# Kernel tuning notes

Hardware: AMD Instinct MI355X
Metric: run time of the kernel (lower is better)

## Reference

```python
import jax, jax.numpy as jnp
import numpy as np

DIM = 384
HEADS = 6
EPS = 1e-5
SCALE = DIM ** -0.5  # note: original uses full dim, not head_dim


def _dwconv_bn(x, w, stride, g, b, m, v):
    # x: [B, C, H, W], w: [C, 1, 3, 3] depthwise
    y = jax.lax.conv_general_dilated(
        x, w, window_strides=(stride, stride), padding=((1, 1), (1, 1)),
        dimension_numbers=('NCHW', 'OIHW', 'NCHW'), feature_group_count=DIM)
    # BatchNorm2d inference form
    inv = jax.lax.rsqrt(v + EPS)
    y = (y - m[None, :, None, None]) * (inv * g)[None, :, None, None] + b[None, :, None, None]
    # b c h w -> b (h w) c
    B, C, H, W = y.shape
    return y.reshape(B, C, H * W).transpose(0, 2, 1)


def setup_inputs() -> dict:
    key = jax.random.key(0)
    ks = jax.random.split(key, 24)
    d = {}
    d['x'] = jax.random.normal(ks[0], (8, 3136, DIM), jnp.float32)
    d['h'] = 56
    d['w'] = 56
    i = 1
    for nm in ('q', 'k', 'v'):
        d[f'conv_{nm}'] = jax.random.normal(ks[i], (DIM, 1, 3, 3), jnp.float32) * 0.1; i += 1
        d[f'bn{nm}_s'] = jnp.ones((DIM,), jnp.float32)
        d[f'bn{nm}_b'] = jnp.zeros((DIM,), jnp.float32)
        d[f'bn{nm}_m'] = jax.random.normal(ks[i], (DIM,), jnp.float32) * 0.1; i += 1
        d[f'bn{nm}_v'] = jax.random.uniform(ks[i], (DIM,), jnp.float32) + 0.5; i += 1
    s = DIM ** -0.5
    d['wq'] = jax.random.normal(ks[i], (DIM, DIM), jnp.float32) * s; i += 1
    d['wk'] = jax.random.normal(ks[i], (DIM, DIM), jnp.float32) * s; i += 1
    d['wv'] = jax.random.normal(ks[i], (DIM, DIM), jnp.float32) * s; i += 1
    d['w_last'] = jax.random.normal(ks[i], (DIM, DIM), jnp.float32) * s; i += 1
    d['b_last'] = jnp.zeros((DIM,), jnp.float32)
    return d


def reference(x, h, w, conv_q, bnq_s, bnq_b, bnq_m, bnq_v,
              conv_k, bnk_s, bnk_b, bnk_m, bnk_v,
              conv_v, bnv_s, bnv_b, bnv_m, bnv_v,
              wq, wk, wv, w_last, b_last):
    B, T, C = x.shape
    xim = x.transpose(0, 2, 1).reshape(B, C, h, w)  # b (h w) c -> b c h w
    q = _dwconv_bn(xim, conv_q, 1, bnq_s, bnq_b, bnq_m, bnq_v)  # [B, h*w, C]
    k = _dwconv_bn(xim, conv_k, 2, bnk_s, bnk_b, bnk_m, bnk_v)  # [B, hw/4, C]
    v = _dwconv_bn(xim, conv_v, 2, bnv_s, bnv_b, bnv_m, bnv_v)
    # linear projections (torch Linear: y = x @ W.T), split heads
    def heads(t, W):
        y = jnp.einsum('btc,oc->bto', t, W)
        Bt, Tt, _ = y.shape
        return y.reshape(Bt, Tt, HEADS, C // HEADS).transpose(0, 2, 1, 3)
    qh, kh, vh = heads(q, wq), heads(k, wk), heads(v, wv)
    attn = jax.nn.softmax(jnp.einsum('bhld,bhtd->bhlt', qh, kh) * SCALE, axis=-1)
    o = jnp.einsum('bhlt,bhtd->bhld', attn, vh)  # [B, H, L, d]
    o = o.transpose(0, 2, 1, 3).reshape(B, T, C)
    return jnp.einsum('btc,oc->bto', o, w_last) + b_last
```

## Files before the change

### kernel.cpp

```cpp
#include <hip/hip_runtime.h>
#include <hip/hip_bf16.h>

typedef __bf16 bf16;
typedef __attribute__((ext_vector_type(8))) __bf16 bf16x8;
typedef __attribute__((ext_vector_type(4))) __bf16 bf16x4;
typedef __attribute__((ext_vector_type(4))) float floatx4;

#define MFMA16(a, b, c) __builtin_amdgcn_mfma_f32_16x16x32_bf16((a), (b), (c), 0, 0, 0)

#define DIM 384
#define T1 3136
#define T2 784
#define T2P 832
#define B_ 8
#define EPSV 1e-5f

__device__ __forceinline__ void gload_lds16(const bf16* g, bf16* l) {
  __builtin_amdgcn_global_load_lds(
      (const __attribute__((address_space(1))) void*)g,
      (__attribute__((address_space(3))) void*)l, 16, 0, 0);
}

__global__ void conv_fused_kernel(const float* __restrict__ x,
    const float* __restrict__ wqc, const float* __restrict__ gq, const float* __restrict__ bq,
    const float* __restrict__ mq, const float* __restrict__ vq,
    const float* __restrict__ wkc, const float* __restrict__ gk, const float* __restrict__ bk,
    const float* __restrict__ mk, const float* __restrict__ vk,
    const float* __restrict__ wvc, const float* __restrict__ gv, const float* __restrict__ bv,
    const float* __restrict__ mv, const float* __restrict__ vvv,
    bf16* __restrict__ qout, bf16* __restrict__ kout, bf16* __restrict__ vout,
    const float* __restrict__ w0, const float* __restrict__ w1,
    const float* __restrict__ w2, const float* __restrict__ w3,
    bf16* __restrict__ d0, bf16* __restrict__ d1,
    bf16* __restrict__ d2, bf16* __restrict__ d3) {
  int blk = blockIdx.x;
  int c = threadIdx.x;
  int gid = blk * DIM + c;
  if (gid < 147456) {
    d0[gid] = (bf16)w0[gid]; d1[gid] = (bf16)w1[gid];
    d2[gid] = (bf16)w2[gid]; d3[gid] = (bf16)w3[gid];
  }
  int xg = blk % 14;
  int y = (blk / 14) % 56;
  int b = blk / (14 * 56);
  int x0 = xg * 4;
  const float* xb = x + (size_t)b * T1 * DIM;
  float in[3][6];
#pragma unroll
  for (int r = 0; r < 3; ++r) {
    int yy = y + r - 1;
#pragma unroll
    for (int cc = 0; cc < 6; ++cc) {
      int xc = x0 + cc - 1;
      in[r][cc] = (yy >= 0 && yy < 56 && xc >= 0 && xc < 56)
                      ? xb[(yy * 56 + xc) * DIM + c] : 0.f;
    }
  }
  {
    float wr[9];
#pragma unroll
    for (int i = 0; i < 9; ++i) wr[i] = wqc[c * 9 + i];
    float a = rsqrtf(vq[c] + EPSV) * gq[c];
    float bia = bq[c] - mq[c] * a;
#pragma unroll
    for (int p = 0; p < 4; ++p) {
      float s = 0.f;
#pragma unroll
      for (int r = 0; r < 3; ++r)
#pragma unroll
        for (int dx = 0; dx < 3; ++dx) s += in[r][p + dx] * wr[r * 3 + dx];
      qout[((size_t)b * T1 + y * 56 + x0 + p) * DIM + c] = (bf16)(s * a + bia);
    }
  }
  if ((y & 1) == 0) {
    int y2 = y >> 1;
    float wk9[9], wv9[9];
#pragma unroll
    for (int i = 0; i < 9; ++i) { wk9[i] = wkc[c * 9 + i]; wv9[i] = wvc[c * 9 + i]; }
    float ak = rsqrtf(vk[c] + EPSV) * gk[c];
    float av = rsqrtf(vvv[c] + EPSV) * gv[c];
    float bik = bk[c] - mk[c] * ak;
    float biv = bv[c] - mv[c] * av;
#pragma unroll
    for (int p2 = 0; p2 < 2; ++p2) {
      float sk = 0.f, sv = 0.f;
#pragma unroll
      for (int r = 0; r < 3; ++r)
#pragma unroll
        for (int dx = 0; dx < 3; ++dx) {
          float xv = in[r][2 * p2 + dx];
          sk += xv * wk9[r * 3 + dx];
          sv += xv * wv9[r * 3 + dx];
        }
      size_t o = ((size_t)b * T2 + y2 * 28 + (x0 >> 1) + p2) * DIM + c;
      kout[o] = (bf16)(sk * ak + bik);
      vout[o] = (bf16)(sv * av + biv);
    }
  }
}

#define BK 32
__device__ __forceinline__
void gemm_body(const bf16* A, const bf16* Bw, void* out, const float* bias,
               int mode, float scale, int m0, int n0, bf16* Al, bf16* Bl) {
  int tid = threadIdx.x;
  int w = tid >> 6, lane = tid & 63;
  int wm = w >> 1, wn = w & 1;
  int l16 = lane & 15, quad = lane >> 4;
  floatx4 acc[4][4];
#pragma unroll
  for (int i = 0; i < 4; ++i)
#pragma unroll
    for (int j = 0; j < 4; ++j) acc[i][j] = (floatx4){0.f, 0.f, 0.f, 0.f};

  int srow = w * 32 + (lane >> 2);
  int scol = (lane & 3) * 8;
  const bf16* ag0 = &A[(size_t)(m0 + srow) * DIM + scol];
  const bf16* ag1 = ag0 + (size_t)16 * DIM;
  const bf16* bg0 = &Bw[(size_t)(n0 + srow) * DIM + scol];
  const bf16* bg1 = bg0 + (size_t)16 * DIM;
  bf16* la0 = &Al[(w * 32) * BK];
  bf16* la1 = &Al[(w * 32 + 16) * BK];
  bf16* lb0 = &Bl[(w * 32) * BK];
  bf16* lb1 = &Bl[(w * 32 + 16) * BK];

  for (int k0 = 0; k0 < DIM; k0 += BK) {
    __syncthreads();
    gload_lds16(ag0 + k0, la0);
    gload_lds16(ag1 + k0, la1);
    gload_lds16(bg0 + k0, lb0);
    gload_lds16(bg1 + k0, lb1);
    __syncthreads();
    bf16x8 af[4], bfr[4];
#pragma unroll
    for (int i = 0; i < 4; ++i) {
      af[i]  = *(const bf16x8*)&Al[(wm * 64 + i * 16 + l16) * BK + quad * 8];
      bfr[i] = *(const bf16x8*)&Bl[(wn * 64 + i * 16 + l16) * BK + quad * 8];
    }
#pragma unroll
    for (int i = 0; i < 4; ++i)
#pragma unroll
      for (int j = 0; j < 4; ++j)
        acc[i][j] = MFMA16(af[i], bfr[j], acc[i][j]);
  }
#pragma unroll
  for (int i = 0; i < 4; ++i) {
#pragma unroll
    for (int j = 0; j < 4; ++j) {
#pragma unroll
      for (int rr = 0; rr < 4; ++rr) {
        int row = m0 + wm * 64 + i * 16 + quad * 4 + rr;
        int col = n0 + wn * 64 + j * 16 + l16;
        float v = acc[i][j][rr];
        if (mode == 3) {
          ((float*)out)[(size_t)row * DIM + col] = v + bias[col];
        } else if (mode == 2) {
          int b = row / T2;
          int t = row - b * T2;
          ((bf16*)out)[((size_t)b * DIM + col) * T2P + t] = (bf16)v;
        } else {
          ((bf16*)out)[(size_t)row * DIM + col] = (bf16)(v * scale);
        }
      }
    }
  }
}

__global__ __launch_bounds__(256)
void qkv_gemm_kernel(const bf16* q_act, const bf16* k_act, const bf16* v_act,
                     const bf16* wqb, const bf16* wkb, const bf16* wvb,
                     bf16* Qp, bf16* Kp, bf16* Vtp, float qscale) {
  __shared__ bf16 Al[128 * BK];
  __shared__ bf16 Bl[128 * BK];
  int bx = blockIdx.x;
  int xp = bx & 7, j = bx >> 3;
  int t = (j / 3) * 24 + xp * 3 + (j % 3);
  if (t >= 882) return;
  const bf16 *A, *Bw; void* out; int mode, ti; float scale;
  if (t < 588)      { A = q_act; Bw = wqb; out = Qp;  mode = 1; scale = qscale; ti = t; }
  else if (t < 735) { A = k_act; Bw = wkb; out = Kp;  mode = 0; scale = 1.f; ti = t - 588; }
  else              { A = v_act; Bw = wvb; out = Vtp; mode = 2; scale = 1.f; ti = t - 735; }
  gemm_body(A, Bw, out, nullptr, mode, scale, (ti / 3) * 128, (ti % 3) * 128, Al, Bl);
}

__global__ __launch_bounds__(256)
void last_gemm_kernel(const bf16* A, const bf16* Bw, float* out, const float* bias) {
  __shared__ bf16 Al[128 * BK];
  __shared__ bf16 Bl[128 * BK];
  int bx = blockIdx.x;
  int xp = bx & 7, j = bx >> 3;
  int t = (j / 3) * 24 + xp * 3 + (j % 3);
  if (t >= 588) return;
  gemm_body(A, Bw, out, bias, 3, 1.f, (t / 3) * 128, (t % 3) * 128, Al, Bl);
}

__global__ __launch_bounds__(256, 4)
void attn_kernel(const bf16* __restrict__ Qp, const bf16* __restrict__ Kp,
                 const bf16* __restrict__ Vt, bf16* __restrict__ Ob) {
  __shared__ bf16 Kl[64 * 64];
  __shared__ bf16 Vl[64 * 64];
  __shared__ bf16 Pl[4][2][16 * 64];
  int bx = blockIdx.x;
  int xcd = bx & 7, j = bx >> 3;
  int g = xcd + 8 * (j / 25);
  int qblk = j % 25;
  int h = g % 6;
  int b = g / 6;
  int tid = threadIdx.x, w = tid >> 6, lane = tid & 63;
  int l16 = lane & 15, quad = lane >> 4;
  int q0w = qblk * 128 + w * 32;

  bf16x8 qf[2][2];
#pragma unroll
  for (int qt = 0; qt < 2; ++qt) {
    int qi = q0w + qt * 16 + l16;
    qi = qi < T1 ? qi : T1 - 1;
    const bf16* qp = &Qp[((size_t)b * T1 + qi) * DIM + h * 64];
    qf[qt][0] = *(const bf16x8*)&qp[quad * 8];
    qf[qt][1] = *(const bf16x8*)&qp[32 + quad * 8];
  }
  floatx4 oacc[2][4];
#pragma unroll
  for (int qt = 0; qt < 2; ++qt)
#pragma unroll
    for (int dt = 0; dt < 4; ++dt) oacc[qt][dt] = (floatx4){0.f, 0.f, 0.f, 0.f};
  float lsum[2] = {0.f, 0.f};

  int rsub = lane >> 3;
  int chnk = (lane & 7) ^ rsub;
  const bf16* kg0 = &Kp[((size_t)b * T2 + w * 16 + rsub) * DIM + h * 64 + chnk * 8];
  const bf16* kg1 = kg0 + (size_t)8 * DIM;
  const bf16* vg0 = &Vt[((size_t)b * DIM + h * 64 + w * 16 + rsub) * T2P + chnk * 8];
  const bf16* vg1 = vg0 + (size_t)8 * T2P;
  bf16* kl0 = &Kl[(w * 16) * 64];
  bf16* kl1 = &Kl[(w * 16 + 8) * 64];
  bf16* vl0 = &Vl[(w * 16) * 64];
  bf16* vl1 = &Vl[(w * 16 + 8) * 64];

  int key = l16 & 7;

  for (int it = 0; it < 12; ++it) {
    __syncthreads();
    gload_lds16(kg0, kl0);
    gload_lds16(kg1, kl1);
    gload_lds16(vg0, vl0);
    gload_lds16(vg1, vl1);
    __syncthreads();
#pragma unroll
    for (int mt = 0; mt < 4; ++mt) {
      int krow = (mt * 16 + l16) * 64;
      bf16x8 kf0 = *(const bf16x8*)&Kl[krow + ((quad) ^ key) * 8];
      bf16x8 kf1 = *(const bf16x8*)&Kl[krow + ((quad + 4) ^ key) * 8];
      int pchunk = (((mt * 2 + (quad >> 1)) ^ key) << 3) + (quad & 1) * 4;
#pragma unroll
      for (int qt = 0; qt < 2; ++qt) {
        floatx4 z = (floatx4){0.f, 0.f, 0.f, 0.f};
        z = MFMA16(kf0, qf[qt][0], z);
        z = MFMA16(kf1, qf[qt][1], z);
        float p0 = __builtin_amdgcn_exp2f(z[0]);
        float p1 = __builtin_amdgcn_exp2f(z[1]);
        float p2 = __builtin_amdgcn_exp2f(z[2]);
        float p3 = __builtin_amdgcn_exp2f(z[3]);
        lsum[qt] += (p0 + p1) + (p2 + p3);
        bf16x4 pw = (bf16x4){(bf16)p0, (bf16)p1, (bf16)p2, (bf16)p3};
        *(bf16x4*)&Pl[w][qt][l16 * 64 + pchunk] = pw;
      }
    }
#pragma unroll
    for (int kt = 0; kt < 2; ++kt) {
      int rchunk = ((kt * 4 + quad) ^ key) << 3;
      bf16x8 pf0 = *(const bf16x8*)&Pl[w][0][l16 * 64 + rchunk];
      bf16x8 pf1 = *(const bf16x8*)&Pl[w][1][l16 * 64 + rchunk];
#pragma unroll
      for (int dt = 0; dt < 4; ++dt) {
        bf16x8 vf = *(const bf16x8*)&Vl[(dt * 16 + l16) * 64 + ((kt * 4 + quad) ^ key) * 8];
        oacc[0][dt] = MFMA16(vf, pf0, oacc[0][dt]);
        oacc[1][dt] = MFMA16(vf, pf1, oacc[1][dt]);
      }
    }
    kg0 += (size_t)64 * DIM; kg1 += (size_t)64 * DIM;
    vg0 += 64; vg1 += 64;
  }
  {
    const bf16* kptr = &Kp[((size_t)b * T2 + 768 + l16) * DIM + h * 64 + quad * 8];
    const bf16* vptr = &Vt[((size_t)b * DIM + h * 64 + l16) * T2P + 768 + quad * 8];
    bf16x8 kf0 = *(const bf16x8*)(kptr);
    bf16x8 kf1 = *(const bf16x8*)(kptr + 32);
    bf16x4 zz = (bf16x4){(bf16)0.f, (bf16)0.f, (bf16)0.f, (bf16)0.f};
    int pc0 = ((((quad >> 1)) ^ key) << 3) + (quad & 1) * 4;
    int pc1 = (((2 + (quad >> 1)) ^ key) << 3) + (quad & 1) * 4;
#pragma unroll
    for (int qt = 0; qt < 2; ++qt) {
      floatx4 z = (floatx4){0.f, 0.f, 0.f, 0.f};
      z = MFMA16(kf0, qf[qt][0], z);
      z = MFMA16(kf1, qf[qt][1], z);
      float p0 = __builtin_amdgcn_exp2f(z[0]);
      float p1 = __builtin_amdgcn_exp2f(z[1]);
      float p2 = __builtin_amdgcn_exp2f(z[2]);
      float p3 = __builtin_amdgcn_exp2f(z[3]);
      lsum[qt] += (p0 + p1) + (p2 + p3);
      bf16x4 pw = (bf16x4){(bf16)p0, (bf16)p1, (bf16)p2, (bf16)p3};
      *(bf16x4*)&Pl[w][qt][l16 * 64 + pc0] = pw;
      *(bf16x4*)&Pl[w][qt][l16 * 64 + pc1] = zz;
    }
    int rchunk = (quad ^ key) << 3;
    bf16x8 pf0 = *(const bf16x8*)&Pl[w][0][l16 * 64 + rchunk];
    bf16x8 pf1 = *(const bf16x8*)&Pl[w][1][l16 * 64 + rchunk];
#pragma unroll
    for (int dt = 0; dt < 4; ++dt) {
      bf16x8 vf = *(const bf16x8*)(vptr + (size_t)(dt * 16) * T2P);
      oacc[0][dt] = MFMA16(vf, pf0, oacc[0][dt]);
      oacc[1][dt] = MFMA16(vf, pf1, oacc[1][dt]);
    }
  }
#pragma unroll
  for (int qt = 0; qt < 2; ++qt) {
    float l = lsum[qt];
    l += __shfl_xor(l, 16);
    l += __shfl_xor(l, 32);
    float inv = 1.f / l;
    int qg = q0w + qt * 16 + l16;
    if (qg < T1) {
      bf16* op = &Ob[((size_t)b * T1 + qg) * DIM + h * 64];
#pragma unroll
      for (int dt = 0; dt < 4; ++dt) {
        floatx4 o = oacc[qt][dt];
        bf16x4 ov = (bf16x4){(bf16)(o[0] * inv), (bf16)(o[1] * inv),
                             (bf16)(o[2] * inv), (bf16)(o[3] * inv)};
        *(bf16x4*)&op[dt * 16 + quad * 4] = ov;
      }
    }
  }
}

extern "C" void kernel_launch(void* const* d_in, const int* in_sizes, int n_in,
                              void* d_out, int out_size, void* d_ws, size_t ws_size,
                              hipStream_t stream) {
  (void)in_sizes; (void)n_in; (void)out_size; (void)ws_size;
  const float* x      = (const float*)d_in[0];
  const float* conv_q = (const float*)d_in[3];
  const float* bnq_s  = (const float*)d_in[4];
  const float* bnq_b  = (const float*)d_in[5];
  const float* bnq_m  = (const float*)d_in[6];
  const float* bnq_v  = (const float*)d_in[7];
  const float* conv_k = (const float*)d_in[8];
  const float* bnk_s  = (const float*)d_in[9];
  const float* bnk_b  = (const float*)d_in[10];
  const float* bnk_m  = (const float*)d_in[11];
  const float* bnk_v  = (const float*)d_in[12];
  const float* conv_v = (const float*)d_in[13];
  const float* bnv_s  = (const float*)d_in[14];
  const float* bnv_b  = (const float*)d_in[15];
  const float* bnv_m  = (const float*)d_in[16];
  const float* bnv_v  = (const float*)d_in[17];
  const float* wq     = (const float*)d_in[18];
  const float* wk     = (const float*)d_in[19];
  const float* wv     = (const float*)d_in[20];
  const float* wl     = (const float*)d_in[21];
  const float* b_last = (const float*)d_in[22];

  char* ws = (char*)d_ws;
  bf16* q_act = (bf16*)(ws + 0);
  bf16* k_act = (bf16*)(ws + 19267584);
  bf16* v_act = (bf16*)(ws + 24084480);
  bf16* Qp    = (bf16*)(ws + 28901376);
  bf16* Kp    = (bf16*)(ws + 48168960);
  bf16* Vtp   = (bf16*)(ws + 52985856);
  bf16* wqb   = (bf16*)(ws + 58097664);
  bf16* wkb   = wqb + 147456;
  bf16* wvb   = wkb + 147456;
  bf16* wlb   = wvb + 147456;

  const float QSCALE = 0.05103103630798288f * 1.4426950408889634f;

  conv_fused_kernel<<<B_ * 56 * 14, DIM, 0, stream>>>(
      x,
      conv_q, bnq_s, bnq_b, bnq_m, bnq_v,
      conv_k, bnk_s, bnk_b, bnk_m, bnk_v,
      conv_v, bnv_s, bnv_b, bnv_m, bnv_v,
      q_act, k_act, v_act,
      wq, wk, wv, wl, wqb, wkb, wvb, wlb);

  qkv_gemm_kernel<<<888, 256, 0, stream>>>(q_act, k_act, v_act, wqb, wkb, wvb,
                                           Qp, Kp, Vtp, QSCALE);

  attn_kernel<<<25 * 6 * B_, 256, 0, stream>>>(Qp, Kp, Vtp, q_act);

  last_gemm_kernel<<<600, 256, 0, stream>>>(q_act, wlb, (float*)d_out, b_last);
}
```

Before: 262.0 us.

## Double-buffer LDS tiles in GEMM body to overlap global loads with MFMA

Turns the shared GEMM body used by the QKV and output projections into a two-stage pipeline. The next K-slice is fetched with global_load_lds into an alternate LDS buffer while the current slice is multiplied, using explicit vmcnt waits and raw s_barrier instead of __syncthreads. The goal is to hide global-load latency behind MFMA work. In exchange the LDS footprint per block doubles, which may lower occupancy, and the hand-written waitcnt and barrier sequence must stay correct.

```diff
diff --git a/kernel.cpp b/kernel.cpp
--- a/kernel.cpp
+++ b/kernel.cpp
@@ -100,6 +100,7 @@
 }
 
 #define BK 32
+#define BUFSZ (128 * BK)
 __device__ __forceinline__
 void gemm_body(const bf16* A, const bf16* Bw, void* out, const float* bias,
                int mode, float scale, int m0, int n0, bf16* Al, bf16* Bl) {
@@ -119,29 +120,46 @@
   const bf16* ag1 = ag0 + (size_t)16 * DIM;
   const bf16* bg0 = &Bw[(size_t)(n0 + srow) * DIM + scol];
   const bf16* bg1 = bg0 + (size_t)16 * DIM;
-  bf16* la0 = &Al[(w * 32) * BK];
-  bf16* la1 = &Al[(w * 32 + 16) * BK];
-  bf16* lb0 = &Bl[(w * 32) * BK];
-  bf16* lb1 = &Bl[(w * 32 + 16) * BK];
-
-  for (int k0 = 0; k0 < DIM; k0 += BK) {
-    __syncthreads();
-    gload_lds16(ag0 + k0, la0);
-    gload_lds16(ag1 + k0, la1);
-    gload_lds16(bg0 + k0, lb0);
-    gload_lds16(bg1 + k0, lb1);
-    __syncthreads();
+  int lofs0 = (w * 32) * BK;
+  int lofs1 = (w * 32 + 16) * BK;
+
+  gload_lds16(ag0, Al + lofs0);
+  gload_lds16(ag1, Al + lofs1);
+  gload_lds16(bg0, Bl + lofs0);
+  gload_lds16(bg1, Bl + lofs1);
+
+  const int NS = DIM / BK;
+#pragma unroll
+  for (int s = 0; s < NS; ++s) {
+    const int cb = s & 1;
+    if (s + 1 < NS) {
+      const int k = (s + 1) * BK;
+      bf16* an = Al + (cb ^ 1) * BUFSZ;
+      bf16* bn = Bl + (cb ^ 1) * BUFSZ;
+      gload_lds16(ag0 + k, an + lofs0);
+      gload_lds16(ag1 + k, an + lofs1);
+      gload_lds16(bg0 + k, bn + lofs0);
+      gload_lds16(bg1 + k, bn + lofs1);
+      asm volatile("s_waitcnt vmcnt(4)" ::: "memory");
+    } else {
+      asm volatile("s_waitcnt vmcnt(0)" ::: "memory");
+    }
+    __builtin_amdgcn_s_barrier();
+    const bf16* Ac = Al + cb * BUFSZ;
+    const bf16* Bc = Bl + cb * BUFSZ;
     bf16x8 af[4], bfr[4];
 #pragma unroll
     for (int i = 0; i < 4; ++i) {
-      af[i]  = *(const bf16x8*)&Al[(wm * 64 + i * 16 + l16) * BK + quad * 8];
-      bfr[i] = *(const bf16x8*)&Bl[(wn * 64 + i * 16 + l16) * BK + quad * 8];
+      af[i]  = *(const bf16x8*)&Ac[(wm * 64 + i * 16 + l16) * BK + quad * 8];
+      bfr[i] = *(const bf16x8*)&Bc[(wn * 64 + i * 16 + l16) * BK + quad * 8];
     }
 #pragma unroll
     for (int i = 0; i < 4; ++i)
 #pragma unroll
       for (int j = 0; j < 4; ++j)
         acc[i][j] = MFMA16(af[i], bfr[j], acc[i][j]);
+    asm volatile("s_waitcnt lgkmcnt(0)" ::: "memory");
+    __builtin_amdgcn_s_barrier();
   }
 #pragma unroll
   for (int i = 0; i < 4; ++i) {
@@ -170,8 +188,8 @@
 void qkv_gemm_kernel(const bf16* q_act, const bf16* k_act, const bf16* v_act,
                      const bf16* wqb, const bf16* wkb, const bf16* wvb,
                      bf16* Qp, bf16* Kp, bf16* Vtp, float qscale) {
-  __shared__ bf16 Al[128 * BK];
-  __shared__ bf16 Bl[128 * BK];
+  __shared__ bf16 Al[2 * BUFSZ];
+  __shared__ bf16 Bl[2 * BUFSZ];
   int bx = blockIdx.x;
   int xp = bx & 7, j = bx >> 3;
   int t = (j / 3) * 24 + xp * 3 + (j % 3);
@@ -185,8 +203,8 @@
 
 __global__ __launch_bounds__(256)
 void last_gemm_kernel(const bf16* A, const bf16* Bw, float* out, const float* bias) {
-  __shared__ bf16 Al[128 * BK];
-  __shared__ bf16 Bl[128 * BK];
+  __shared__ bf16 Al[2 * BUFSZ];
+  __shared__ bf16 Bl[2 * BUFSZ];
   int bx = blockIdx.x;
   int xp = bx & 7, j = bx >> 3;
   int t = (j / 3) * 24 + xp * 3 + (j % 3);
```

Result: faster. 248.3 us (-5.2%).
